# Optimization experiments

Hardware: AMD Instinct MI355X
Metric: run time of the kernel (lower is better)

Reference implementation:

```python
import jax, jax.numpy as jnp
import numpy as np

N_NODES = 100000

def gin_conv(x, edge_index, W, b):
    # PyG GINConv with eps=0: out = Linear(x + sum_{j->i} x_j)
    src, dst = edge_index[0], edge_index[1]
    agg = jax.ops.segment_sum(x[src], dst, num_segments=N_NODES)  # [N, d]
    return (x + agg) @ W + b

def setup_inputs() -> dict:
    key = jax.random.key(0)
    ks = jax.random.split(key, 8)
    x = jax.random.normal(ks[0], (N_NODES, 32), dtype=jnp.float32)
    edge_index = jax.random.randint(ks[1], (2, 1600000), 0, N_NODES, dtype=jnp.int64)
    def lin(k, fan_in, fan_out):
        kw, kb = jax.random.split(k)
        lim = 1.0 / np.sqrt(fan_in)
        W = jax.random.uniform(kw, (fan_in, fan_out), minval=-lim, maxval=lim, dtype=jnp.float32)
        b = jax.random.uniform(kb, (fan_out,), minval=-lim, maxval=lim, dtype=jnp.float32)
        return W, b
    W1, b1 = lin(ks[2], 32, 64)
    W2, b2 = lin(ks[3], 64, 64)
    W3, b3 = lin(ks[4], 64, 10)
    return {"x": x, "edge_index": edge_index,
            "W1": W1, "b1": b1, "W2": W2, "b2": b2, "W3": W3, "b3": b3}

def reference(x, edge_index, W1, b1, W2, b2, W3, b3):
    h = jax.nn.relu(gin_conv(x, edge_index, W1, b1))
    h = jax.nn.relu(gin_conv(h, edge_index, W2, b2))
    return gin_conv(h, edge_index, W3, b3)  # [N, classes] logits
```

## Files before the change

### kernel.cpp

```cpp
#include <hip/hip_runtime.h>


#define GIN_N 100000
#define NBUCKET 256
#define NB2 391
#define BSTRIDE 8192
#define EPT 16

typedef float v2f __attribute__((ext_vector_type(2)));
typedef float f32x4 __attribute__((ext_vector_type(4)));
typedef short s16x8 __attribute__((ext_vector_type(8)));
typedef unsigned int u32x4 __attribute__((ext_vector_type(4)));

__device__ __forceinline__ float bf_lo(unsigned int u) {
    return __uint_as_float(u << 16);
}
__device__ __forceinline__ float bf_hi(unsigned int u) {
    return __uint_as_float(u & 0xffff0000u);
}
__device__ __forceinline__ unsigned int f2bf(float f) {
    unsigned int u = __float_as_uint(f);
    return (u + 0x7fffu + ((u >> 16) & 1u)) >> 16;
}
__device__ __forceinline__ unsigned pk2bf(float lo, float hi) {
    return f2bf(lo) | (f2bf(hi) << 16);
}
__device__ __forceinline__ v2f fp8lo(unsigned u) {
    return __builtin_amdgcn_cvt_pk_f32_fp8(u, false);
}
__device__ __forceinline__ v2f fp8hi(unsigned u) {
    return __builtin_amdgcn_cvt_pk_f32_fp8(u, true);
}
__device__ __forceinline__ s16x8 lds_frag(const unsigned* p) {
    return __builtin_bit_cast(s16x8, *reinterpret_cast<const u32x4*>(p));
}

template <int S>
__device__ __forceinline__ void blelloch_excl(int* a) {
#pragma unroll
    for (int d = 1; d < S; d <<= 1) {
        __syncthreads();
        int idx = (threadIdx.x + 1) * (d << 1) - 1;
        if (idx < S) a[idx] += a[idx - d];
    }
    __syncthreads();
    if (threadIdx.x == 0) a[S - 1] = 0;
#pragma unroll
    for (int d = S >> 1; d >= 1; d >>= 1) {
        __syncthreads();
        int idx = (threadIdx.x + 1) * (d << 1) - 1;
        if (idx < S) {
            int t = a[idx - d];
            a[idx - d] = a[idx];
            a[idx] += t;
        }
    }
    __syncthreads();
}

__global__ __launch_bounds__(256) void build_kernel(
        const int* __restrict__ src, const int* __restrict__ dst, int E,
        unsigned* __restrict__ bucketbuf, int* __restrict__ cursor,
        const float* __restrict__ x, unsigned* __restrict__ xq, int n8,
        int bblk) {
    __shared__ int h[NBUCKET];
    __shared__ int base[NBUCKET];
    int tid = threadIdx.x;
    if (blockIdx.x >= bblk) {
        int t = (blockIdx.x - bblk) * 256 + tid;
        if (t == 0) {
            uint4 z = make_uint4(0, 0, 0, 0);
            reinterpret_cast<uint4*>(xq + (size_t)GIN_N * 8)[0] = z;
            reinterpret_cast<uint4*>(xq + (size_t)GIN_N * 8)[1] = z;
        }
        if (t >= n8) return;
        const float4* v = reinterpret_cast<const float4*>(x);
        float4 a = v[2 * t], b = v[2 * t + 1];
        unsigned w0 = 0, w1 = 0;
        w0 = __builtin_amdgcn_cvt_pk_fp8_f32(a.x, a.y, w0, false);
        w0 = __builtin_amdgcn_cvt_pk_fp8_f32(a.z, a.w, w0, true);
        w1 = __builtin_amdgcn_cvt_pk_fp8_f32(b.x, b.y, w1, false);
        w1 = __builtin_amdgcn_cvt_pk_fp8_f32(b.z, b.w, w1, true);
        reinterpret_cast<uint2*>(xq)[t] = make_uint2(w0, w1);
        return;
    }
    int chunk0 = blockIdx.x * (256 * EPT);
    h[tid] = 0;
    __syncthreads();
    unsigned mybr[EPT];
    unsigned myrec[EPT];
#pragma unroll
    for (int i = 0; i < EPT; ++i) {
        int e = chunk0 + tid + i * 256;
        if (e < E) {
            int d = dst[e];
            int s = src[e];
            int b = d / NB2;
            int rank = atomicAdd(&h[b], 1);
            mybr[i] = ((unsigned)rank << 8) | (unsigned)b;
            myrec[i] = ((unsigned)(d - b * NB2) << 17) | (unsigned)s;
        } else {
            mybr[i] = 0xFFFFFFFFu;
        }
    }
    __syncthreads();
    base[tid] = atomicAdd(&cursor[tid], h[tid]);
    __syncthreads();
#pragma unroll
    for (int i = 0; i < EPT; ++i) {
        if (mybr[i] == 0xFFFFFFFFu) continue;
        int b = (int)(mybr[i] & 0xFFu);
        int pos = base[b] + (int)(mybr[i] >> 8);
        if (pos < BSTRIDE) bucketbuf[(size_t)b * BSTRIDE + pos] = myrec[i];
    }
}

__global__ __launch_bounds__(1024) void csr_build_kernel(
        const unsigned* __restrict__ bucketbuf,
        const int* __restrict__ cursor,
        int* __restrict__ rowptr,
        int* __restrict__ deg,
        int* __restrict__ adj) {
    __shared__ int csr[BSTRIDE];
    __shared__ int cnt[512];
    __shared__ int off[512];
    __shared__ int bscan[NBUCKET];
    __shared__ int tot;
    int b = blockIdx.x;
    int tid = threadIdx.x;
    if (tid < NBUCKET) {
        int c = cursor[tid];
        if (c > BSTRIDE) c = BSTRIDE;
        bscan[tid] = (c + 3 * NB2 + 3) & ~3;
    }
    int mycnt = cursor[b];
    if (mycnt > BSTRIDE) mycnt = BSTRIDE;
    blelloch_excl<NBUCKET>(bscan);
    int base = bscan[b];

    const unsigned* buf = bucketbuf + (size_t)b * BSTRIDE;
    if (tid < 512) cnt[tid] = 0;
    __syncthreads();
    for (int i = tid; i < mycnt; i += 1024)
        atomicAdd(&cnt[buf[i] >> 17], 1);
    __syncthreads();
    if (tid < 512) off[tid] = (cnt[tid] + 3) & ~3;
    blelloch_excl<512>(off);
    if (tid == 0) tot = off[511] + ((cnt[511] + 3) & ~3);

    int nodes0 = b * NB2;
    int nn2 = GIN_N + 1 - nodes0;
    if (nn2 > NB2) nn2 = NB2;
    int nnode = GIN_N - nodes0;
    if (nnode > NB2) nnode = NB2;
    for (int l = tid; l < nn2; l += 1024) rowptr[nodes0 + l] = base + off[l];
    for (int l = tid; l < nnode; l += 1024) {
        deg[nodes0 + l] = cnt[l];
        int s = off[l] + cnt[l];
        int e2 = off[l] + ((cnt[l] + 3) & ~3);
        for (int p = s; p < e2; ++p)
            if (p < BSTRIDE) csr[p] = GIN_N;
    }
    __syncthreads();

    for (int i = tid; i < mycnt; i += 1024) {
        unsigned r = buf[i];
        int pos = atomicAdd(&off[r >> 17], 1);
        if (pos < BSTRIDE) csr[pos] = (int)(r & 0x1FFFFu);
    }
    __syncthreads();
    int T = tot;
    if (T > BSTRIDE) T = BSTRIDE;
    for (int i = tid; i < T; i += 1024) adj[base + i] = csr[i];
}

__global__ __launch_bounds__(256, 8) void fused1_kernel(
        const float* __restrict__ xf,
        const unsigned* __restrict__ xq,
        const int* __restrict__ rowptr,
        const int* __restrict__ deg,
        const int* __restrict__ adj,
        const float* __restrict__ W,
        const float* __restrict__ b,
        unsigned* __restrict__ outq) {
    constexpr int K = 32, M = 64;
    constexpr int TPN = 4, NODES = 64;
    constexpr int KW = K / 2;
    constexpr int WSTR = KW + 4;

    __shared__ unsigned Wb[M * WSTR];
    __shared__ float bs[M];
    __shared__ unsigned tile[NODES * WSTR];

    int tid = threadIdx.x;
    if (blockIdx.x == 0 && tid < 4) {
        reinterpret_cast<uint4*>(outq + (size_t)GIN_N * 16)[tid] =
            make_uint4(0, 0, 0, 0);
    }
    for (int i = tid; i < M * KW; i += 256) {
        int k2 = i >> 6, j = i & 63;
        Wb[j * WSTR + k2] = pk2bf(W[(2 * k2) * M + j], W[(2 * k2 + 1) * M + j]);
    }
    if (tid < M) bs[tid] = b[tid];

    int node0 = blockIdx.x * NODES;

    {
        int l = tid / TPN;
        int j = tid % TPN;
        int n = node0 + l;
        if (n < GIN_N) {
            int start = rowptr[n];
            int n4 = (deg[n] + 3) >> 2;
            const int4* row4 = reinterpret_cast<const int4*>(adj + start);
            const uint2* fq = reinterpret_cast<const uint2*>(xq);
            v2f a0, a1, a2, a3;
            {
                const float4* xv = reinterpret_cast<const float4*>(xf);
                float4 a = xv[(size_t)n * 8 + 2 * j];
                float4 c = xv[(size_t)n * 8 + 2 * j + 1];
                a0 = v2f{a.x, a.y}; a1 = v2f{a.z, a.w};
                a2 = v2f{c.x, c.y}; a3 = v2f{c.z, c.w};
            }
#define ACC8(v) { a0 += fp8lo(v.x); a1 += fp8hi(v.x); \
                  a2 += fp8lo(v.y); a3 += fp8hi(v.y); }
            int q = 0;
            for (; q + 2 <= n4; q += 2) {
                int4 ra = row4[q], rb = row4[q + 1];
                uint2 v0 = fq[(size_t)ra.x * 4 + j];
                uint2 v1 = fq[(size_t)ra.y * 4 + j];
                uint2 v2 = fq[(size_t)ra.z * 4 + j];
                uint2 v3 = fq[(size_t)ra.w * 4 + j];
                uint2 v4 = fq[(size_t)rb.x * 4 + j];
                uint2 v5 = fq[(size_t)rb.y * 4 + j];
                uint2 v6 = fq[(size_t)rb.z * 4 + j];
                uint2 v7 = fq[(size_t)rb.w * 4 + j];
                ACC8(v0) ACC8(v1) ACC8(v2) ACC8(v3)
                ACC8(v4) ACC8(v5) ACC8(v6) ACC8(v7)
            }
            if (q < n4) {
                int4 ra = row4[q];
                uint2 v0 = fq[(size_t)ra.x * 4 + j];
                uint2 v1 = fq[(size_t)ra.y * 4 + j];
                uint2 v2 = fq[(size_t)ra.z * 4 + j];
                uint2 v3 = fq[(size_t)ra.w * 4 + j];
                ACC8(v0) ACC8(v1) ACC8(v2) ACC8(v3)
            }
#undef ACC8
            *reinterpret_cast<uint4*>(&tile[l * WSTR + j * 4]) = make_uint4(
                pk2bf(a0.x, a0.y), pk2bf(a1.x, a1.y),
                pk2bf(a2.x, a2.y), pk2bf(a3.x, a3.y));
        }
    }
    __syncthreads();

    {
        int w = tid >> 6;
        int l = tid & 63;
        int c = l & 15;
        int g = l >> 4;
        int n = node0 + w * 16 + c;
        s16x8 bf = lds_frag(&tile[(w * 16 + c) * WSTR + 4 * g]);
#pragma unroll
        for (int jt = 0; jt < 4; ++jt) {
            int j0 = jt * 16;
            s16x8 af = lds_frag(&Wb[(j0 + c) * WSTR + 4 * g]);
            f32x4 a;
            a.x = bs[j0 + 4 * g + 0];
            a.y = bs[j0 + 4 * g + 1];
            a.z = bs[j0 + 4 * g + 2];
            a.w = bs[j0 + 4 * g + 3];
            a = __builtin_amdgcn_mfma_f32_16x16x32_bf16(af, bf, a, 0, 0, 0);
            float r0 = fmaxf(a.x, 0.0f), r1 = fmaxf(a.y, 0.0f);
            float r2 = fmaxf(a.z, 0.0f), r3 = fmaxf(a.w, 0.0f);
            unsigned u = 0;
            u = __builtin_amdgcn_cvt_pk_fp8_f32(r0, r1, u, false);
            u = __builtin_amdgcn_cvt_pk_fp8_f32(r2, r3, u, true);
            if (n < GIN_N) outq[(size_t)n * 16 + jt * 4 + g] = u;
        }
    }
}

__global__ __launch_bounds__(256, 8) void fused2t_kernel(
        const unsigned* __restrict__ xq,
        const int* __restrict__ rowptr,
        const int* __restrict__ deg,
        const int* __restrict__ adj,
        const float* __restrict__ W,
        const float* __restrict__ b,
        const float* __restrict__ W3,
        unsigned* __restrict__ tout) {
    constexpr int K = 64, M = 64;
    constexpr int TPN = 8, NODES = 32;
    constexpr int KW = K / 2;
    constexpr int WSTR = KW + 4;

    __shared__ unsigned Wb[M * WSTR];
    __shared__ float bs[M];
    __shared__ float W3n[M * 12];
    __shared__ unsigned tile[NODES * WSTR];
    __shared__ float ptb[2][NODES][10];

    int tid = threadIdx.x;
    if (blockIdx.x == 0 && tid < 2) {
        reinterpret_cast<uint4*>(tout + (size_t)GIN_N * 8)[tid] =
            make_uint4(0, 0, 0, 0);
    }
    for (int i = tid; i < M * KW; i += 256) {
        int k2 = i >> 6, j = i & 63;
        Wb[j * WSTR + k2] = pk2bf(W[(2 * k2) * M + j], W[(2 * k2 + 1) * M + j]);
    }
    for (int i = tid; i < M * 10; i += 256) {
        int j = i / 10, jj = i - 10 * j;
        W3n[j * 12 + jj] = W3[i];
    }
    if (tid < M) bs[tid] = b[tid];

    int node0 = blockIdx.x * NODES;

    {
        int l = tid / TPN;
        int j = tid % TPN;
        int n = node0 + l;
        if (n < GIN_N) {
            int start = rowptr[n];
            int n4 = (deg[n] + 3) >> 2;
            const int4* row4 = reinterpret_cast<const int4*>(adj + start);
            const uint2* fq = reinterpret_cast<const uint2*>(xq);
            v2f a0, a1, a2, a3;
            {
                uint2 s = fq[(size_t)n * 8 + j];
                a0 = fp8lo(s.x); a1 = fp8hi(s.x);
                a2 = fp8lo(s.y); a3 = fp8hi(s.y);
            }
#define ACC8(v) { a0 += fp8lo(v.x); a1 += fp8hi(v.x); \
                  a2 += fp8lo(v.y); a3 += fp8hi(v.y); }
            int q = 0;
            for (; q + 2 <= n4; q += 2) {
                int4 ra = row4[q], rb = row4[q + 1];
                uint2 v0 = fq[(size_t)ra.x * 8 + j];
                uint2 v1 = fq[(size_t)ra.y * 8 + j];
                uint2 v2 = fq[(size_t)ra.z * 8 + j];
                uint2 v3 = fq[(size_t)ra.w * 8 + j];
                uint2 v4 = fq[(size_t)rb.x * 8 + j];
                uint2 v5 = fq[(size_t)rb.y * 8 + j];
                uint2 v6 = fq[(size_t)rb.z * 8 + j];
                uint2 v7 = fq[(size_t)rb.w * 8 + j];
                ACC8(v0) ACC8(v1) ACC8(v2) ACC8(v3)
                ACC8(v4) ACC8(v5) ACC8(v6) ACC8(v7)
            }
            if (q < n4) {
                int4 ra = row4[q];
                uint2 v0 = fq[(size_t)ra.x * 8 + j];
                uint2 v1 = fq[(size_t)ra.y * 8 + j];
                uint2 v2 = fq[(size_t)ra.z * 8 + j];
                uint2 v3 = fq[(size_t)ra.w * 8 + j];
                ACC8(v0) ACC8(v1) ACC8(v2) ACC8(v3)
            }
#undef ACC8
            *reinterpret_cast<uint4*>(&tile[l * WSTR + j * 4]) = make_uint4(
                pk2bf(a0.x, a0.y), pk2bf(a1.x, a1.y),
                pk2bf(a2.x, a2.y), pk2bf(a3.x, a3.y));
        }
    }
    __syncthreads();

    {
        int w  = tid >> 6;
        int l  = tid & 63;
        int c  = l & 15;
        int g  = l >> 4;
        int nt = w & 1;
        int jp = w >> 1;
        const unsigned* trow = &tile[(nt * 16 + c) * WSTR];
        s16x8 bf0 = lds_frag(trow + 4 * g);
        s16x8 bf1 = lds_frag(trow + 16 + 4 * g);
        f32x4 acc[2];
#pragma unroll
        for (int jt = 0; jt < 2; ++jt) {
            int j0 = (2 * jp + jt) * 16;
            const unsigned* arow = &Wb[(j0 + c) * WSTR];
            s16x8 af0 = lds_frag(arow + 4 * g);
            s16x8 af1 = lds_frag(arow + 16 + 4 * g);
            f32x4 a;
            a.x = bs[j0 + 4 * g + 0];
            a.y = bs[j0 + 4 * g + 1];
            a.z = bs[j0 + 4 * g + 2];
            a.w = bs[j0 + 4 * g + 3];
            a = __builtin_amdgcn_mfma_f32_16x16x32_bf16(af0, bf0, a, 0, 0, 0);
            a = __builtin_amdgcn_mfma_f32_16x16x32_bf16(af1, bf1, a, 0, 0, 0);
            acc[jt] = a;
        }
        v2f pt[5];
#pragma unroll
        for (int q = 0; q < 5; ++q) pt[q] = v2f{0.0f, 0.0f};
#pragma unroll
        for (int jt = 0; jt < 2; ++jt) {
            int jb = (2 * jp + jt) * 16 + 4 * g;
#pragma unroll
            for (int r = 0; r < 4; ++r) {
                float h = fmaxf(acc[jt][r], 0.0f);
                const v2f* wr =
                    reinterpret_cast<const v2f*>(&W3n[(jb + r) * 12]);
#pragma unroll
                for (int q = 0; q < 5; ++q) pt[q] += wr[q] * h;
            }
        }
        float ptf[10];
#pragma unroll
        for (int q = 0; q < 5; ++q) { ptf[2 * q] = pt[q].x; ptf[2 * q + 1] = pt[q].y; }
#pragma unroll
        for (int jj = 0; jj < 10; ++jj) {
            float v = ptf[jj];
            v += __shfl_xor(v, 16, 64);
            v += __shfl_xor(v, 32, 64);
            ptf[jj] = v;
        }
        if (g == 0) {
#pragma unroll
            for (int jj = 0; jj < 10; ++jj)
                ptb[jp][nt * 16 + c][jj] = ptf[jj];
        }
    }
    __syncthreads();

    {
        int n = tid >> 3, q = tid & 7;
        int node = node0 + n;
        unsigned u = 0;
        if (q < 5) {
            float lo = ptb[0][n][2 * q]     + ptb[1][n][2 * q];
            float hi = ptb[0][n][2 * q + 1] + ptb[1][n][2 * q + 1];
            u = pk2bf(lo, hi);
        }
        if (node < GIN_N) tout[(size_t)node * 8 + q] = u;
    }
}

__global__ __launch_bounds__(256) void gather_final_kernel(
        const unsigned* __restrict__ t8,
        const int* __restrict__ rowptr,
        const int* __restrict__ deg,
        const int* __restrict__ adj,
        const float* __restrict__ b3,
        float* __restrict__ out) {
    int t = blockIdx.x * blockDim.x + threadIdx.x;
    int n = t / 5;
    int j = t - n * 5;
    if (n >= GIN_N) return;
    int start = rowptr[n];
    int n4 = (deg[n] + 3) >> 2;
    const int4* row4 = reinterpret_cast<const int4*>(adj + start);
    unsigned sv = t8[(size_t)n * 8 + j];
    float a0 = bf_lo(sv), a1 = bf_hi(sv);
    int q = 0;
    for (; q + 2 <= n4; q += 2) {
        int4 ra = row4[q], rb = row4[q + 1];
        unsigned v0 = t8[(size_t)ra.x * 8 + j];
        unsigned v1 = t8[(size_t)ra.y * 8 + j];
        unsigned v2 = t8[(size_t)ra.z * 8 + j];
        unsigned v3 = t8[(size_t)ra.w * 8 + j];
        unsigned v4 = t8[(size_t)rb.x * 8 + j];
        unsigned v5 = t8[(size_t)rb.y * 8 + j];
        unsigned v6 = t8[(size_t)rb.z * 8 + j];
        unsigned v7 = t8[(size_t)rb.w * 8 + j];
        a0 += bf_lo(v0) + bf_lo(v1) + bf_lo(v2) + bf_lo(v3);
        a1 += bf_hi(v0) + bf_hi(v1) + bf_hi(v2) + bf_hi(v3);
        a0 += bf_lo(v4) + bf_lo(v5) + bf_lo(v6) + bf_lo(v7);
        a1 += bf_hi(v4) + bf_hi(v5) + bf_hi(v6) + bf_hi(v7);
    }
    if (q < n4) {
        int4 ra = row4[q];
        unsigned v0 = t8[(size_t)ra.x * 8 + j];
        unsigned v1 = t8[(size_t)ra.y * 8 + j];
        unsigned v2 = t8[(size_t)ra.z * 8 + j];
        unsigned v3 = t8[(size_t)ra.w * 8 + j];
        a0 += bf_lo(v0) + bf_lo(v1) + bf_lo(v2) + bf_lo(v3);
        a1 += bf_hi(v0) + bf_hi(v1) + bf_hi(v2) + bf_hi(v3);
    }
    const float2* b2v = reinterpret_cast<const float2*>(b3);
    float2 bb = b2v[j];
    float2 r; r.x = a0 + bb.x; r.y = a1 + bb.y;
    *reinterpret_cast<float2*>(out + (size_t)n * 10 + 2 * j) = r;
}

extern "C" void kernel_launch(void* const* d_in, const int* in_sizes, int n_in,
                              void* d_out, int out_size, void* d_ws, size_t ws_size,
                              hipStream_t stream) {
    const float* x  = (const float*)d_in[0];
    const int*   ei = (const int*)d_in[1];
    const float* W1 = (const float*)d_in[2];
    const float* b1 = (const float*)d_in[3];
    const float* W2 = (const float*)d_in[4];
    const float* b2 = (const float*)d_in[5];
    const float* W3 = (const float*)d_in[6];
    const float* b3 = (const float*)d_in[7];
    float* out = (float*)d_out;

    const int N = GIN_N;
    const int E = in_sizes[1] / 2;
    const int* src = ei;
    const int* dst = ei + E;

    unsigned* Xq = (unsigned*)d_ws;
    unsigned* H1q = Xq + (size_t)(N + 1) * 8;
    unsigned* Tb = H1q + (size_t)(N + 1) * 16;
    int* rowptr = (int*)(Tb + (size_t)(N + 1) * 8);
    int* deg = rowptr + (N + 8);
    int* cursor = deg + (N + 8);
    int* adj = cursor + 256;
    unsigned* bucketbuf = (unsigned*)(adj + (size_t)E + 256 * (3 * NB2 + 4));

    const int BLK = 256;

    hipMemsetAsync(cursor, 0, 256 * sizeof(int), stream);

    {
        int n8 = N * 32 / 8;
        int bblk = (E + BLK * EPT - 1) / (BLK * EPT);
        int xblk = (n8 + BLK - 1) / BLK;
        build_kernel<<<bblk + xblk, BLK, 0, stream>>>(
            src, dst, E, bucketbuf, cursor, x, Xq, n8, bblk);
        csr_build_kernel<<<NBUCKET, 1024, 0, stream>>>(
            bucketbuf, cursor, rowptr, deg, adj);
    }

    fused1_kernel<<<(N + 63) / 64, BLK, 0, stream>>>(
        x, Xq, rowptr, deg, adj, W1, b1, H1q);

    fused2t_kernel<<<(N + 31) / 32, BLK, 0, stream>>>(
        H1q, rowptr, deg, adj, W2, b2, W3, Tb);

    gather_final_kernel<<<(N * 5 + BLK - 1) / BLK, BLK, 0, stream>>>(
        Tb, rowptr, deg, adj, b3, out);
}
```

Before: 179.4 us.

## Widen gather loads to 16 bytes and split edge lists across thread pairs

All three gather kernels now fetch neighbour features as 16-byte uint4 loads instead of 8-byte or 4-byte loads, with fewer threads per feature row. In fused1 and gather_final, two threads per row split the adjacency list into alternating quads and combine partial sums with a cross-lane shuffle. fused2t now has each wave compute all 64 hidden outputs for its 16 nodes, which removes the cross-wave partial-sum LDS buffer and the extra barrier and writes the output row directly. Blocks grow to 512 threads and 128 nodes. The intent is fewer memory transactions per edge, at the cost of more registers per thread and less thread-level parallelism per node.

```diff
diff --git a/kernel.cpp b/kernel.cpp
--- a/kernel.cpp
+++ b/kernel.cpp
@@ -174,7 +174,7 @@
     for (int i = tid; i < T; i += 1024) adj[base + i] = csr[i];
 }
 
-__global__ __launch_bounds__(256, 8) void fused1_kernel(
+__global__ __launch_bounds__(512, 8) void fused1_kernel(
         const float* __restrict__ xf,
         const unsigned* __restrict__ xq,
         const int* __restrict__ rowptr,
@@ -184,7 +184,7 @@
         const float* __restrict__ b,
         unsigned* __restrict__ outq) {
     constexpr int K = 32, M = 64;
-    constexpr int TPN = 4, NODES = 64;
+    constexpr int NODES = 128;
     constexpr int KW = K / 2;
     constexpr int WSTR = KW + 4;
 
@@ -197,7 +197,7 @@
         reinterpret_cast<uint4*>(outq + (size_t)GIN_N * 16)[tid] =
             make_uint4(0, 0, 0, 0);
     }
-    for (int i = tid; i < M * KW; i += 256) {
+    for (int i = tid; i < M * KW; i += 512) {
         int k2 = i >> 6, j = i & 63;
         Wb[j * WSTR + k2] = pk2bf(W[(2 * k2) * M + j], W[(2 * k2 + 1) * M + j]);
     }
@@ -206,50 +206,54 @@
     int node0 = blockIdx.x * NODES;
 
     {
-        int l = tid / TPN;
-        int j = tid % TPN;
+        int l = tid >> 2;
+        int j = tid & 1;
+        int h = (tid >> 1) & 1;
         int n = node0 + l;
         if (n < GIN_N) {
             int start = rowptr[n];
             int n4 = (deg[n] + 3) >> 2;
             const int4* row4 = reinterpret_cast<const int4*>(adj + start);
-            const uint2* fq = reinterpret_cast<const uint2*>(xq);
-            v2f a0, a1, a2, a3;
-            {
+            const uint4* fq4 = reinterpret_cast<const uint4*>(xq);
+            v2f a[8];
+            if (h == 0) {
                 const float4* xv = reinterpret_cast<const float4*>(xf);
-                float4 a = xv[(size_t)n * 8 + 2 * j];
-                float4 c = xv[(size_t)n * 8 + 2 * j + 1];
-                a0 = v2f{a.x, a.y}; a1 = v2f{a.z, a.w};
-                a2 = v2f{c.x, c.y}; a3 = v2f{c.z, c.w};
-            }
-#define ACC8(v) { a0 += fp8lo(v.x); a1 += fp8hi(v.x); \
-                  a2 += fp8lo(v.y); a3 += fp8hi(v.y); }
-            int q = 0;
-            for (; q + 2 <= n4; q += 2) {
-                int4 ra = row4[q], rb = row4[q + 1];
-                uint2 v0 = fq[(size_t)ra.x * 4 + j];
-                uint2 v1 = fq[(size_t)ra.y * 4 + j];
-                uint2 v2 = fq[(size_t)ra.z * 4 + j];
-                uint2 v3 = fq[(size_t)ra.w * 4 + j];
-                uint2 v4 = fq[(size_t)rb.x * 4 + j];
-                uint2 v5 = fq[(size_t)rb.y * 4 + j];
-                uint2 v6 = fq[(size_t)rb.z * 4 + j];
-                uint2 v7 = fq[(size_t)rb.w * 4 + j];
-                ACC8(v0) ACC8(v1) ACC8(v2) ACC8(v3)
-                ACC8(v4) ACC8(v5) ACC8(v6) ACC8(v7)
-            }
-            if (q < n4) {
+#pragma unroll
+                for (int p = 0; p < 4; ++p) {
+                    float4 s = xv[(size_t)n * 8 + 4 * j + p];
+                    a[2 * p]     = v2f{s.x, s.y};
+                    a[2 * p + 1] = v2f{s.z, s.w};
+                }
+            } else {
+#pragma unroll
+                for (int p = 0; p < 8; ++p) a[p] = v2f{0.0f, 0.0f};
+            }
+#define ACC16(v) { a[0] += fp8lo(v.x); a[1] += fp8hi(v.x); \
+                   a[2] += fp8lo(v.y); a[3] += fp8hi(v.y); \
+                   a[4] += fp8lo(v.z); a[5] += fp8hi(v.z); \
+                   a[6] += fp8lo(v.w); a[7] += fp8hi(v.w); }
+            for (int q = h; q < n4; q += 2) {
                 int4 ra = row4[q];
-                uint2 v0 = fq[(size_t)ra.x * 4 + j];
-                uint2 v1 = fq[(size_t)ra.y * 4 + j];
-                uint2 v2 = fq[(size_t)ra.z * 4 + j];
-                uint2 v3 = fq[(size_t)ra.w * 4 + j];
-                ACC8(v0) ACC8(v1) ACC8(v2) ACC8(v3)
-            }
-#undef ACC8
-            *reinterpret_cast<uint4*>(&tile[l * WSTR + j * 4]) = make_uint4(
-                pk2bf(a0.x, a0.y), pk2bf(a1.x, a1.y),
-                pk2bf(a2.x, a2.y), pk2bf(a3.x, a3.y));
+                uint4 v0 = fq4[(size_t)ra.x * 2 + j];
+                uint4 v1 = fq4[(size_t)ra.y * 2 + j];
+                uint4 v2 = fq4[(size_t)ra.z * 2 + j];
+                uint4 v3 = fq4[(size_t)ra.w * 2 + j];
+                ACC16(v0) ACC16(v1) ACC16(v2) ACC16(v3)
+            }
+#undef ACC16
+#pragma unroll
+            for (int p = 0; p < 8; ++p) {
+                a[p].x += __shfl_xor(a[p].x, 2, 64);
+                a[p].y += __shfl_xor(a[p].y, 2, 64);
+            }
+            if (h == 0) {
+                *reinterpret_cast<uint4*>(&tile[l * WSTR + j * 8]) =
+                    make_uint4(pk2bf(a[0].x, a[0].y), pk2bf(a[1].x, a[1].y),
+                               pk2bf(a[2].x, a[2].y), pk2bf(a[3].x, a[3].y));
+                *reinterpret_cast<uint4*>(&tile[l * WSTR + j * 8 + 4]) =
+                    make_uint4(pk2bf(a[4].x, a[4].y), pk2bf(a[5].x, a[5].y),
+                               pk2bf(a[6].x, a[6].y), pk2bf(a[7].x, a[7].y));
+            }
         }
     }
     __syncthreads();
@@ -281,7 +285,7 @@
     }
 }
 
-__global__ __launch_bounds__(256, 8) void fused2t_kernel(
+__global__ __launch_bounds__(512, 8) void fused2t_kernel(
         const unsigned* __restrict__ xq,
         const int* __restrict__ rowptr,
         const int* __restrict__ deg,
@@ -291,7 +295,7 @@
         const float* __restrict__ W3,
         unsigned* __restrict__ tout) {
     constexpr int K = 64, M = 64;
-    constexpr int TPN = 8, NODES = 32;
+    constexpr int NODES = 128;
     constexpr int KW = K / 2;
     constexpr int WSTR = KW + 4;
 
@@ -299,18 +303,17 @@
     __shared__ float bs[M];
     __shared__ float W3n[M * 12];
     __shared__ unsigned tile[NODES * WSTR];
-    __shared__ float ptb[2][NODES][10];
 
     int tid = threadIdx.x;
     if (blockIdx.x == 0 && tid < 2) {
         reinterpret_cast<uint4*>(tout + (size_t)GIN_N * 8)[tid] =
             make_uint4(0, 0, 0, 0);
     }
-    for (int i = tid; i < M * KW; i += 256) {
+    for (int i = tid; i < M * KW; i += 512) {
         int k2 = i >> 6, j = i & 63;
         Wb[j * WSTR + k2] = pk2bf(W[(2 * k2) * M + j], W[(2 * k2 + 1) * M + j]);
     }
-    for (int i = tid; i < M * 10; i += 256) {
+    for (int i = tid; i < M * 10; i += 512) {
         int j = i / 10, jj = i - 10 * j;
         W3n[j * 12 + jj] = W3[i];
     }
@@ -319,66 +322,60 @@
     int node0 = blockIdx.x * NODES;
 
     {
-        int l = tid / TPN;
-        int j = tid % TPN;
+        int l = tid >> 2;
+        int j = tid & 3;
         int n = node0 + l;
         if (n < GIN_N) {
             int start = rowptr[n];
             int n4 = (deg[n] + 3) >> 2;
             const int4* row4 = reinterpret_cast<const int4*>(adj + start);
-            const uint2* fq = reinterpret_cast<const uint2*>(xq);
-            v2f a0, a1, a2, a3;
+            const uint4* fq4 = reinterpret_cast<const uint4*>(xq);
+            v2f a[8];
             {
-                uint2 s = fq[(size_t)n * 8 + j];
-                a0 = fp8lo(s.x); a1 = fp8hi(s.x);
-                a2 = fp8lo(s.y); a3 = fp8hi(s.y);
-            }
-#define ACC8(v) { a0 += fp8lo(v.x); a1 += fp8hi(v.x); \
-                  a2 += fp8lo(v.y); a3 += fp8hi(v.y); }
-            int q = 0;
-            for (; q + 2 <= n4; q += 2) {
-                int4 ra = row4[q], rb = row4[q + 1];
-                uint2 v0 = fq[(size_t)ra.x * 8 + j];
-                uint2 v1 = fq[(size_t)ra.y * 8 + j];
-                uint2 v2 = fq[(size_t)ra.z * 8 + j];
-                uint2 v3 = fq[(size_t)ra.w * 8 + j];
-                uint2 v4 = fq[(size_t)rb.x * 8 + j];
-                uint2 v5 = fq[(size_t)rb.y * 8 + j];
-                uint2 v6 = fq[(size_t)rb.z * 8 + j];
-                uint2 v7 = fq[(size_t)rb.w * 8 + j];
-                ACC8(v0) ACC8(v1) ACC8(v2) ACC8(v3)
-                ACC8(v4) ACC8(v5) ACC8(v6) ACC8(v7)
-            }
-            if (q < n4) {
+                uint4 s = fq4[(size_t)n * 4 + j];
+                a[0] = fp8lo(s.x); a[1] = fp8hi(s.x);
+                a[2] = fp8lo(s.y); a[3] = fp8hi(s.y);
+                a[4] = fp8lo(s.z); a[5] = fp8hi(s.z);
+                a[6] = fp8lo(s.w); a[7] = fp8hi(s.w);
+            }
+#define ACC16(v) { a[0] += fp8lo(v.x); a[1] += fp8hi(v.x); \
+                   a[2] += fp8lo(v.y); a[3] += fp8hi(v.y); \
+                   a[4] += fp8lo(v.z); a[5] += fp8hi(v.z); \
+                   a[6] += fp8lo(v.w); a[7] += fp8hi(v.w); }
+            for (int q = 0; q < n4; ++q) {
                 int4 ra = row4[q];
-                uint2 v0 = fq[(size_t)ra.x * 8 + j];
-                uint2 v1 = fq[(size_t)ra.y * 8 + j];
-                uint2 v2 = fq[(size_t)ra.z * 8 + j];
-                uint2 v3 = fq[(size_t)ra.w * 8 + j];
-                ACC8(v0) ACC8(v1) ACC8(v2) ACC8(v3)
-            }
-#undef ACC8
-            *reinterpret_cast<uint4*>(&tile[l * WSTR + j * 4]) = make_uint4(
-                pk2bf(a0.x, a0.y), pk2bf(a1.x, a1.y),
-                pk2bf(a2.x, a2.y), pk2bf(a3.x, a3.y));
+                uint4 v0 = fq4[(size_t)ra.x * 4 + j];
+                uint4 v1 = fq4[(size_t)ra.y * 4 + j];
+                uint4 v2 = fq4[(size_t)ra.z * 4 + j];
+                uint4 v3 = fq4[(size_t)ra.w * 4 + j];
+                ACC16(v0) ACC16(v1) ACC16(v2) ACC16(v3)
+            }
+#undef ACC16
+            *reinterpret_cast<uint4*>(&tile[l * WSTR + j * 8]) =
+                make_uint4(pk2bf(a[0].x, a[0].y), pk2bf(a[1].x, a[1].y),
+                           pk2bf(a[2].x, a[2].y), pk2bf(a[3].x, a[3].y));
+            *reinterpret_cast<uint4*>(&tile[l * WSTR + j * 8 + 4]) =
+                make_uint4(pk2bf(a[4].x, a[4].y), pk2bf(a[5].x, a[5].y),
+                           pk2bf(a[6].x, a[6].y), pk2bf(a[7].x, a[7].y));
         }
     }
     __syncthreads();
 
     {
-        int w  = tid >> 6;
-        int l  = tid & 63;
-        int c  = l & 15;
-        int g  = l >> 4;
-        int nt = w & 1;
-        int jp = w >> 1;
-        const unsigned* trow = &tile[(nt * 16 + c) * WSTR];
+        int w = tid >> 6;
+        int l = tid & 63;
+        int c = l & 15;
+        int g = l >> 4;
+        int n = node0 + w * 16 + c;
+        const unsigned* trow = &tile[(w * 16 + c) * WSTR];
         s16x8 bf0 = lds_frag(trow + 4 * g);
         s16x8 bf1 = lds_frag(trow + 16 + 4 * g);
-        f32x4 acc[2];
-#pragma unroll
-        for (int jt = 0; jt < 2; ++jt) {
-            int j0 = (2 * jp + jt) * 16;
+        v2f pt[5];
+#pragma unroll
+        for (int q = 0; q < 5; ++q) pt[q] = v2f{0.0f, 0.0f};
+#pragma unroll
+        for (int jt = 0; jt < 4; ++jt) {
+            int j0 = jt * 16;
             const unsigned* arow = &Wb[(j0 + c) * WSTR];
             s16x8 af0 = lds_frag(arow + 4 * g);
             s16x8 af1 = lds_frag(arow + 16 + 4 * g);
@@ -389,21 +386,13 @@
             a.w = bs[j0 + 4 * g + 3];
             a = __builtin_amdgcn_mfma_f32_16x16x32_bf16(af0, bf0, a, 0, 0, 0);
             a = __builtin_amdgcn_mfma_f32_16x16x32_bf16(af1, bf1, a, 0, 0, 0);
-            acc[jt] = a;
-        }
-        v2f pt[5];
-#pragma unroll
-        for (int q = 0; q < 5; ++q) pt[q] = v2f{0.0f, 0.0f};
-#pragma unroll
-        for (int jt = 0; jt < 2; ++jt) {
-            int jb = (2 * jp + jt) * 16 + 4 * g;
 #pragma unroll
             for (int r = 0; r < 4; ++r) {
-                float h = fmaxf(acc[jt][r], 0.0f);
+                float hh = fmaxf(a[r], 0.0f);
                 const v2f* wr =
-                    reinterpret_cast<const v2f*>(&W3n[(jb + r) * 12]);
-#pragma unroll
-                for (int q = 0; q < 5; ++q) pt[q] += wr[q] * h;
+                    reinterpret_cast<const v2f*>(&W3n[(j0 + 4 * g + r) * 12]);
+#pragma unroll
+                for (int q = 0; q < 5; ++q) pt[q] += wr[q] * hh;
             }
         }
         float ptf[10];
@@ -416,28 +405,16 @@
             v += __shfl_xor(v, 32, 64);
             ptf[jj] = v;
         }
-        if (g == 0) {
-#pragma unroll
-            for (int jj = 0; jj < 10; ++jj)
-                ptb[jp][nt * 16 + c][jj] = ptf[jj];
-        }
-    }
-    __syncthreads();
-
-    {
-        int n = tid >> 3, q = tid & 7;
-        int node = node0 + n;
-        unsigned u = 0;
-        if (q < 5) {
-            float lo = ptb[0][n][2 * q]     + ptb[1][n][2 * q];
-            float hi = ptb[0][n][2 * q + 1] + ptb[1][n][2 * q + 1];
-            u = pk2bf(lo, hi);
-        }
-        if (node < GIN_N) tout[(size_t)node * 8 + q] = u;
-    }
-}
-
-__global__ __launch_bounds__(256) void gather_final_kernel(
+        if (g == 0 && n < GIN_N) {
+            uint4* o = reinterpret_cast<uint4*>(tout + (size_t)n * 8);
+            o[0] = make_uint4(pk2bf(ptf[0], ptf[1]), pk2bf(ptf[2], ptf[3]),
+                              pk2bf(ptf[4], ptf[5]), pk2bf(ptf[6], ptf[7]));
+            o[1] = make_uint4(pk2bf(ptf[8], ptf[9]), 0, 0, 0);
+        }
+    }
+}
+
+__global__ __launch_bounds__(256, 8) void gather_final_kernel(
         const unsigned* __restrict__ t8,
         const int* __restrict__ rowptr,
         const int* __restrict__ deg,
@@ -445,43 +422,57 @@
         const float* __restrict__ b3,
         float* __restrict__ out) {
     int t = blockIdx.x * blockDim.x + threadIdx.x;
-    int n = t / 5;
-    int j = t - n * 5;
+    int n = t >> 2;
     if (n >= GIN_N) return;
+    int j = t & 1;
+    int h = (t >> 1) & 1;
     int start = rowptr[n];
     int n4 = (deg[n] + 3) >> 2;
     const int4* row4 = reinterpret_cast<const int4*>(adj + start);
-    unsigned sv = t8[(size_t)n * 8 + j];
-    float a0 = bf_lo(sv), a1 = bf_hi(sv);
-    int q = 0;
-    for (; q + 2 <= n4; q += 2) {
-        int4 ra = row4[q], rb = row4[q + 1];
-        unsigned v0 = t8[(size_t)ra.x * 8 + j];
-        unsigned v1 = t8[(size_t)ra.y * 8 + j];
-        unsigned v2 = t8[(size_t)ra.z * 8 + j];
-        unsigned v3 = t8[(size_t)ra.w * 8 + j];
-        unsigned v4 = t8[(size_t)rb.x * 8 + j];
-        unsigned v5 = t8[(size_t)rb.y * 8 + j];
-        unsigned v6 = t8[(size_t)rb.z * 8 + j];
-        unsigned v7 = t8[(size_t)rb.w * 8 + j];
-        a0 += bf_lo(v0) + bf_lo(v1) + bf_lo(v2) + bf_lo(v3);
-        a1 += bf_hi(v0) + bf_hi(v1) + bf_hi(v2) + bf_hi(v3);
-        a0 += bf_lo(v4) + bf_lo(v5) + bf_lo(v6) + bf_lo(v7);
-        a1 += bf_hi(v4) + bf_hi(v5) + bf_hi(v6) + bf_hi(v7);
-    }
-    if (q < n4) {
+    const uint4* t4 = reinterpret_cast<const uint4*>(t8);
+    v2f a[4];
+    if (h == 0) {
+        uint4 s = t4[(size_t)n * 2 + j];
+        a[0] = v2f{bf_lo(s.x), bf_hi(s.x)};
+        a[1] = v2f{bf_lo(s.y), bf_hi(s.y)};
+        a[2] = v2f{bf_lo(s.z), bf_hi(s.z)};
+        a[3] = v2f{bf_lo(s.w), bf_hi(s.w)};
+    } else {
+#pragma unroll
+        for (int p = 0; p < 4; ++p) a[p] = v2f{0.0f, 0.0f};
+    }
+#define ACCT(v) { a[0] += v2f{bf_lo(v.x), bf_hi(v.x)}; \
+                  a[1] += v2f{bf_lo(v.y), bf_hi(v.y)}; \
+                  a[2] += v2f{bf_lo(v.z), bf_hi(v.z)}; \
+                  a[3] += v2f{bf_lo(v.w), bf_hi(v.w)}; }
+    for (int q = h; q < n4; q += 2) {
         int4 ra = row4[q];
-        unsigned v0 = t8[(size_t)ra.x * 8 + j];
-        unsigned v1 = t8[(size_t)ra.y * 8 + j];
-        unsigned v2 = t8[(size_t)ra.z * 8 + j];
-        unsigned v3 = t8[(size_t)ra.w * 8 + j];
-        a0 += bf_lo(v0) + bf_lo(v1) + bf_lo(v2) + bf_lo(v3);
-        a1 += bf_hi(v0) + bf_hi(v1) + bf_hi(v2) + bf_hi(v3);
-    }
-    const float2* b2v = reinterpret_cast<const float2*>(b3);
-    float2 bb = b2v[j];
-    float2 r; r.x = a0 + bb.x; r.y = a1 + bb.y;
-    *reinterpret_cast<float2*>(out + (size_t)n * 10 + 2 * j) = r;
+        uint4 v0 = t4[(size_t)ra.x * 2 + j];
+        uint4 v1 = t4[(size_t)ra.y * 2 + j];
+        uint4 v2 = t4[(size_t)ra.z * 2 + j];
+        uint4 v3 = t4[(size_t)ra.w * 2 + j];
+        ACCT(v0) ACCT(v1) ACCT(v2) ACCT(v3)
+    }
+#undef ACCT
+#pragma unroll
+    for (int p = 0; p < 4; ++p) {
+        a[p].x += __shfl_xor(a[p].x, 2, 64);
+        a[p].y += __shfl_xor(a[p].y, 2, 64);
+    }
+    if (h == 0) {
+        if (j == 0) {
+#pragma unroll
+            for (int p = 0; p < 4; ++p) {
+                float2 bb = reinterpret_cast<const float2*>(b3)[p];
+                float2 r; r.x = a[p].x + bb.x; r.y = a[p].y + bb.y;
+                *reinterpret_cast<float2*>(out + (size_t)n * 10 + 2 * p) = r;
+            }
+        } else {
+            float2 bb = reinterpret_cast<const float2*>(b3)[4];
+            float2 r; r.x = a[0].x + bb.x; r.y = a[0].y + bb.y;
+            *reinterpret_cast<float2*>(out + (size_t)n * 10 + 8) = r;
+        }
+    }
 }
 
 extern "C" void kernel_launch(void* const* d_in, const int* in_sizes, int n_in,
@@ -525,12 +516,12 @@
             bucketbuf, cursor, rowptr, deg, adj);
     }
 
-    fused1_kernel<<<(N + 63) / 64, BLK, 0, stream>>>(
+    fused1_kernel<<<(N + 127) / 128, 512, 0, stream>>>(
         x, Xq, rowptr, deg, adj, W1, b1, H1q);
 
-    fused2t_kernel<<<(N + 31) / 32, BLK, 0, stream>>>(
+    fused2t_kernel<<<(N + 127) / 128, 512, 0, stream>>>(
         H1q, rowptr, deg, adj, W2, b2, W3, Tb);
 
-    gather_final_kernel<<<(N * 5 + BLK - 1) / BLK, BLK, 0, stream>>>(
+    gather_final_kernel<<<(N * 4 + BLK - 1) / BLK, BLK, 0, stream>>>(
         Tb, rowptr, deg, adj, b3, out);
 }
```

Result: slower. 194.6 us (+8.5%).

## Double threads per node in fused gather kernels, splitting features into 4-byte slices

Applied to the files above, without the earlier changes.

Both fused gather+MLP kernels move from 256 to 512 threads per block and assign twice as many threads per node, so each thread gathers one 32-bit fp8 word per neighbor instead of a uint2. This raises memory-level parallelism for the irregular neighbor gathers and halves per-thread register accumulators. The MFMA stage is redistributed over 8 waves, with fused2t reducing the layer-3 partial products over four column groups instead of two. The trade-off is narrower per-thread loads, meaning more load instructions per byte, plus more threads issuing the same index loads.

```diff
diff --git a/kernel.cpp b/kernel.cpp
--- a/kernel.cpp
+++ b/kernel.cpp
@@ -174,7 +174,7 @@
     for (int i = tid; i < T; i += 1024) adj[base + i] = csr[i];
 }
 
-__global__ __launch_bounds__(256, 8) void fused1_kernel(
+__global__ __launch_bounds__(512, 8) void fused1_kernel(
         const float* __restrict__ xf,
         const unsigned* __restrict__ xq,
         const int* __restrict__ rowptr,
@@ -184,7 +184,7 @@
         const float* __restrict__ b,
         unsigned* __restrict__ outq) {
     constexpr int K = 32, M = 64;
-    constexpr int TPN = 4, NODES = 64;
+    constexpr int NODES = 64;
     constexpr int KW = K / 2;
     constexpr int WSTR = KW + 4;
 
@@ -197,7 +197,7 @@
         reinterpret_cast<uint4*>(outq + (size_t)GIN_N * 16)[tid] =
             make_uint4(0, 0, 0, 0);
     }
-    for (int i = tid; i < M * KW; i += 256) {
+    for (int i = tid; i < M * KW; i += 512) {
         int k2 = i >> 6, j = i & 63;
         Wb[j * WSTR + k2] = pk2bf(W[(2 * k2) * M + j], W[(2 * k2 + 1) * M + j]);
     }
@@ -206,50 +206,44 @@
     int node0 = blockIdx.x * NODES;
 
     {
-        int l = tid / TPN;
-        int j = tid % TPN;
+        int l = tid >> 3;
+        int j = tid & 7;
         int n = node0 + l;
         if (n < GIN_N) {
             int start = rowptr[n];
             int n4 = (deg[n] + 3) >> 2;
             const int4* row4 = reinterpret_cast<const int4*>(adj + start);
-            const uint2* fq = reinterpret_cast<const uint2*>(xq);
-            v2f a0, a1, a2, a3;
+            v2f a0, a1;
             {
-                const float4* xv = reinterpret_cast<const float4*>(xf);
-                float4 a = xv[(size_t)n * 8 + 2 * j];
-                float4 c = xv[(size_t)n * 8 + 2 * j + 1];
-                a0 = v2f{a.x, a.y}; a1 = v2f{a.z, a.w};
-                a2 = v2f{c.x, c.y}; a3 = v2f{c.z, c.w};
+                float4 s = reinterpret_cast<const float4*>(xf)[(size_t)n * 8 + j];
+                a0 = v2f{s.x, s.y}; a1 = v2f{s.z, s.w};
             }
-#define ACC8(v) { a0 += fp8lo(v.x); a1 += fp8hi(v.x); \
-                  a2 += fp8lo(v.y); a3 += fp8hi(v.y); }
+#define ACC4(v) { a0 += fp8lo(v); a1 += fp8hi(v); }
             int q = 0;
             for (; q + 2 <= n4; q += 2) {
                 int4 ra = row4[q], rb = row4[q + 1];
-                uint2 v0 = fq[(size_t)ra.x * 4 + j];
-                uint2 v1 = fq[(size_t)ra.y * 4 + j];
-                uint2 v2 = fq[(size_t)ra.z * 4 + j];
-                uint2 v3 = fq[(size_t)ra.w * 4 + j];
-                uint2 v4 = fq[(size_t)rb.x * 4 + j];
-                uint2 v5 = fq[(size_t)rb.y * 4 + j];
-                uint2 v6 = fq[(size_t)rb.z * 4 + j];
-                uint2 v7 = fq[(size_t)rb.w * 4 + j];
-                ACC8(v0) ACC8(v1) ACC8(v2) ACC8(v3)
-                ACC8(v4) ACC8(v5) ACC8(v6) ACC8(v7)
+                unsigned v0 = xq[(size_t)ra.x * 8 + j];
+                unsigned v1 = xq[(size_t)ra.y * 8 + j];
+                unsigned v2 = xq[(size_t)ra.z * 8 + j];
+                unsigned v3 = xq[(size_t)ra.w * 8 + j];
+                unsigned v4 = xq[(size_t)rb.x * 8 + j];
+                unsigned v5 = xq[(size_t)rb.y * 8 + j];
+                unsigned v6 = xq[(size_t)rb.z * 8 + j];
+                unsigned v7 = xq[(size_t)rb.w * 8 + j];
+                ACC4(v0) ACC4(v1) ACC4(v2) ACC4(v3)
+                ACC4(v4) ACC4(v5) ACC4(v6) ACC4(v7)
             }
             if (q < n4) {
                 int4 ra = row4[q];
-                uint2 v0 = fq[(size_t)ra.x * 4 + j];
-                uint2 v1 = fq[(size_t)ra.y * 4 + j];
-                uint2 v2 = fq[(size_t)ra.z * 4 + j];
-                uint2 v3 = fq[(size_t)ra.w * 4 + j];
-                ACC8(v0) ACC8(v1) ACC8(v2) ACC8(v3)
+                unsigned v0 = xq[(size_t)ra.x * 8 + j];
+                unsigned v1 = xq[(size_t)ra.y * 8 + j];
+                unsigned v2 = xq[(size_t)ra.z * 8 + j];
+                unsigned v3 = xq[(size_t)ra.w * 8 + j];
+                ACC4(v0) ACC4(v1) ACC4(v2) ACC4(v3)
             }
-#undef ACC8
-            *reinterpret_cast<uint4*>(&tile[l * WSTR + j * 4]) = make_uint4(
-                pk2bf(a0.x, a0.y), pk2bf(a1.x, a1.y),
-                pk2bf(a2.x, a2.y), pk2bf(a3.x, a3.y));
+#undef ACC4
+            *reinterpret_cast<uint2*>(&tile[l * WSTR + 2 * j]) =
+                make_uint2(pk2bf(a0.x, a0.y), pk2bf(a1.x, a1.y));
         }
     }
     __syncthreads();
@@ -259,11 +253,13 @@
         int l = tid & 63;
         int c = l & 15;
         int g = l >> 4;
-        int n = node0 + w * 16 + c;
-        s16x8 bf = lds_frag(&tile[(w * 16 + c) * WSTR + 4 * g]);
-#pragma unroll
-        for (int jt = 0; jt < 4; ++jt) {
-            int j0 = jt * 16;
+        int nt = w >> 1;
+        int jp = w & 1;
+        int n = node0 + nt * 16 + c;
+        s16x8 bf = lds_frag(&tile[(nt * 16 + c) * WSTR + 4 * g]);
+#pragma unroll
+        for (int jt = 0; jt < 2; ++jt) {
+            int j0 = (2 * jp + jt) * 16;
             s16x8 af = lds_frag(&Wb[(j0 + c) * WSTR + 4 * g]);
             f32x4 a;
             a.x = bs[j0 + 4 * g + 0];
@@ -276,12 +272,12 @@
             unsigned u = 0;
             u = __builtin_amdgcn_cvt_pk_fp8_f32(r0, r1, u, false);
             u = __builtin_amdgcn_cvt_pk_fp8_f32(r2, r3, u, true);
-            if (n < GIN_N) outq[(size_t)n * 16 + jt * 4 + g] = u;
-        }
-    }
-}
-
-__global__ __launch_bounds__(256, 8) void fused2t_kernel(
+            if (n < GIN_N) outq[(size_t)n * 16 + (2 * jp + jt) * 4 + g] = u;
+        }
+    }
+}
+
+__global__ __launch_bounds__(512, 8) void fused2t_kernel(
         const unsigned* __restrict__ xq,
         const int* __restrict__ rowptr,
         const int* __restrict__ deg,
@@ -291,7 +287,7 @@
         const float* __restrict__ W3,
         unsigned* __restrict__ tout) {
     constexpr int K = 64, M = 64;
-    constexpr int TPN = 8, NODES = 32;
+    constexpr int NODES = 32;
     constexpr int KW = K / 2;
     constexpr int WSTR = KW + 4;
 
@@ -299,18 +295,18 @@
     __shared__ float bs[M];
     __shared__ float W3n[M * 12];
     __shared__ unsigned tile[NODES * WSTR];
-    __shared__ float ptb[2][NODES][10];
+    __shared__ float ptb[4][NODES][10];
 
     int tid = threadIdx.x;
     if (blockIdx.x == 0 && tid < 2) {
         reinterpret_cast<uint4*>(tout + (size_t)GIN_N * 8)[tid] =
             make_uint4(0, 0, 0, 0);
     }
-    for (int i = tid; i < M * KW; i += 256) {
+    for (int i = tid; i < M * KW; i += 512) {
         int k2 = i >> 6, j = i & 63;
         Wb[j * WSTR + k2] = pk2bf(W[(2 * k2) * M + j], W[(2 * k2 + 1) * M + j]);
     }
-    for (int i = tid; i < M * 10; i += 256) {
+    for (int i = tid; i < M * 10; i += 512) {
         int j = i / 10, jj = i - 10 * j;
         W3n[j * 12 + jj] = W3[i];
     }
@@ -319,48 +315,44 @@
     int node0 = blockIdx.x * NODES;
 
     {
-        int l = tid / TPN;
-        int j = tid % TPN;
+        int l = tid >> 4;
+        int j = tid & 15;
         int n = node0 + l;
         if (n < GIN_N) {
             int start = rowptr[n];
             int n4 = (deg[n] + 3) >> 2;
             const int4* row4 = reinterpret_cast<const int4*>(adj + start);
-            const uint2* fq = reinterpret_cast<const uint2*>(xq);
-            v2f a0, a1, a2, a3;
+            v2f a0, a1;
             {
-                uint2 s = fq[(size_t)n * 8 + j];
-                a0 = fp8lo(s.x); a1 = fp8hi(s.x);
-                a2 = fp8lo(s.y); a3 = fp8hi(s.y);
+                unsigned s = xq[(size_t)n * 16 + j];
+                a0 = fp8lo(s); a1 = fp8hi(s);
             }
-#define ACC8(v) { a0 += fp8lo(v.x); a1 += fp8hi(v.x); \
-                  a2 += fp8lo(v.y); a3 += fp8hi(v.y); }
+#define ACC4(v) { a0 += fp8lo(v); a1 += fp8hi(v); }
             int q = 0;
             for (; q + 2 <= n4; q += 2) {
                 int4 ra = row4[q], rb = row4[q + 1];
-                uint2 v0 = fq[(size_t)ra.x * 8 + j];
-                uint2 v1 = fq[(size_t)ra.y * 8 + j];
-                uint2 v2 = fq[(size_t)ra.z * 8 + j];
-                uint2 v3 = fq[(size_t)ra.w * 8 + j];
-                uint2 v4 = fq[(size_t)rb.x * 8 + j];
-                uint2 v5 = fq[(size_t)rb.y * 8 + j];
-                uint2 v6 = fq[(size_t)rb.z * 8 + j];
-                uint2 v7 = fq[(size_t)rb.w * 8 + j];
-                ACC8(v0) ACC8(v1) ACC8(v2) ACC8(v3)
-                ACC8(v4) ACC8(v5) ACC8(v6) ACC8(v7)
+                unsigned v0 = xq[(size_t)ra.x * 16 + j];
+                unsigned v1 = xq[(size_t)ra.y * 16 + j];
+                unsigned v2 = xq[(size_t)ra.z * 16 + j];
+                unsigned v3 = xq[(size_t)ra.w * 16 + j];
+                unsigned v4 = xq[(size_t)rb.x * 16 + j];
+                unsigned v5 = xq[(size_t)rb.y * 16 + j];
+                unsigned v6 = xq[(size_t)rb.z * 16 + j];
+                unsigned v7 = xq[(size_t)rb.w * 16 + j];
+                ACC4(v0) ACC4(v1) ACC4(v2) ACC4(v3)
+                ACC4(v4) ACC4(v5) ACC4(v6) ACC4(v7)
             }
             if (q < n4) {
                 int4 ra = row4[q];
-                uint2 v0 = fq[(size_t)ra.x * 8 + j];
-                uint2 v1 = fq[(size_t)ra.y * 8 + j];
-                uint2 v2 = fq[(size_t)ra.z * 8 + j];
-                uint2 v3 = fq[(size_t)ra.w * 8 + j];
-                ACC8(v0) ACC8(v1) ACC8(v2) ACC8(v3)
+                unsigned v0 = xq[(size_t)ra.x * 16 + j];
+                unsigned v1 = xq[(size_t)ra.y * 16 + j];
+                unsigned v2 = xq[(size_t)ra.z * 16 + j];
+                unsigned v3 = xq[(size_t)ra.w * 16 + j];
+                ACC4(v0) ACC4(v1) ACC4(v2) ACC4(v3)
             }
-#undef ACC8
-            *reinterpret_cast<uint4*>(&tile[l * WSTR + j * 4]) = make_uint4(
-                pk2bf(a0.x, a0.y), pk2bf(a1.x, a1.y),
-                pk2bf(a2.x, a2.y), pk2bf(a3.x, a3.y));
+#undef ACC4
+            *reinterpret_cast<uint2*>(&tile[l * WSTR + 2 * j]) =
+                make_uint2(pk2bf(a0.x, a0.y), pk2bf(a1.x, a1.y));
         }
     }
     __syncthreads();
@@ -370,41 +362,32 @@
         int l  = tid & 63;
         int c  = l & 15;
         int g  = l >> 4;
-        int nt = w & 1;
-        int jp = w >> 1;
+        int nt = w >> 2;
+        int jw = w & 3;
         const unsigned* trow = &tile[(nt * 16 + c) * WSTR];
         s16x8 bf0 = lds_frag(trow + 4 * g);
         s16x8 bf1 = lds_frag(trow + 16 + 4 * g);
-        f32x4 acc[2];
-#pragma unroll
-        for (int jt = 0; jt < 2; ++jt) {
-            int j0 = (2 * jp + jt) * 16;
-            const unsigned* arow = &Wb[(j0 + c) * WSTR];
-            s16x8 af0 = lds_frag(arow + 4 * g);
-            s16x8 af1 = lds_frag(arow + 16 + 4 * g);
-            f32x4 a;
-            a.x = bs[j0 + 4 * g + 0];
-            a.y = bs[j0 + 4 * g + 1];
-            a.z = bs[j0 + 4 * g + 2];
-            a.w = bs[j0 + 4 * g + 3];
-            a = __builtin_amdgcn_mfma_f32_16x16x32_bf16(af0, bf0, a, 0, 0, 0);
-            a = __builtin_amdgcn_mfma_f32_16x16x32_bf16(af1, bf1, a, 0, 0, 0);
-            acc[jt] = a;
-        }
+        int j0 = jw * 16;
+        const unsigned* arow = &Wb[(j0 + c) * WSTR];
+        s16x8 af0 = lds_frag(arow + 4 * g);
+        s16x8 af1 = lds_frag(arow + 16 + 4 * g);
+        f32x4 a;
+        a.x = bs[j0 + 4 * g + 0];
+        a.y = bs[j0 + 4 * g + 1];
+        a.z = bs[j0 + 4 * g + 2];
+        a.w = bs[j0 + 4 * g + 3];
+        a = __builtin_amdgcn_mfma_f32_16x16x32_bf16(af0, bf0, a, 0, 0, 0);
+        a = __builtin_amdgcn_mfma_f32_16x16x32_bf16(af1, bf1, a, 0, 0, 0);
         v2f pt[5];
 #pragma unroll
         for (int q = 0; q < 5; ++q) pt[q] = v2f{0.0f, 0.0f};
 #pragma unroll
-        for (int jt = 0; jt < 2; ++jt) {
-            int jb = (2 * jp + jt) * 16 + 4 * g;
-#pragma unroll
-            for (int r = 0; r < 4; ++r) {
-                float h = fmaxf(acc[jt][r], 0.0f);
-                const v2f* wr =
-                    reinterpret_cast<const v2f*>(&W3n[(jb + r) * 12]);
-#pragma unroll
-                for (int q = 0; q < 5; ++q) pt[q] += wr[q] * h;
-            }
+        for (int r = 0; r < 4; ++r) {
+            float hh = fmaxf(a[r], 0.0f);
+            const v2f* wr =
+                reinterpret_cast<const v2f*>(&W3n[(j0 + 4 * g + r) * 12]);
+#pragma unroll
+            for (int q = 0; q < 5; ++q) pt[q] += wr[q] * hh;
         }
         float ptf[10];
 #pragma unroll
@@ -419,18 +402,20 @@
         if (g == 0) {
 #pragma unroll
             for (int jj = 0; jj < 10; ++jj)
-                ptb[jp][nt * 16 + c][jj] = ptf[jj];
-        }
-    }
-    __syncthreads();
-
-    {
+                ptb[jw][nt * 16 + c][jj] = ptf[jj];
+        }
+    }
+    __syncthreads();
+
+    if (tid < NODES * 8) {
         int n = tid >> 3, q = tid & 7;
         int node = node0 + n;
         unsigned u = 0;
         if (q < 5) {
-            float lo = ptb[0][n][2 * q]     + ptb[1][n][2 * q];
-            float hi = ptb[0][n][2 * q + 1] + ptb[1][n][2 * q + 1];
+            float lo = ptb[0][n][2 * q] + ptb[1][n][2 * q]
+                     + ptb[2][n][2 * q] + ptb[3][n][2 * q];
+            float hi = ptb[0][n][2 * q + 1] + ptb[1][n][2 * q + 1]
+                     + ptb[2][n][2 * q + 1] + ptb[3][n][2 * q + 1];
             u = pk2bf(lo, hi);
         }
         if (node < GIN_N) tout[(size_t)node * 8 + q] = u;
@@ -525,10 +510,10 @@
             bucketbuf, cursor, rowptr, deg, adj);
     }
 
-    fused1_kernel<<<(N + 63) / 64, BLK, 0, stream>>>(
+    fused1_kernel<<<(N + 63) / 64, 512, 0, stream>>>(
         x, Xq, rowptr, deg, adj, W1, b1, H1q);
 
-    fused2t_kernel<<<(N + 31) / 32, BLK, 0, stream>>>(
+    fused2t_kernel<<<(N + 31) / 32, 512, 0, stream>>>(
         H1q, rowptr, deg, adj, W2, b2, W3, Tb);
 
     gather_final_kernel<<<(N * 5 + BLK - 1) / BLK, BLK, 0, stream>>>(
```

Measured after the change: 182.8 us. No clear change (+1.9%).
